# Optimization experiments

Measured on AMD Instinct MI355X. Metric: run time of the kernel, lower is better.

The kernel has to match this reference:

```python
import jax, jax.numpy as jnp
import numpy as np

B, L, E, H = 2, 2048, 1024, 16
D = E // H

def setup_inputs() -> dict:
    key = jax.random.key(0)
    ks = jax.random.split(key, 6)
    values = jax.random.normal(ks[0], (B, L, E), dtype=jnp.float32)
    keys = jax.random.normal(ks[1], (B, L, E), dtype=jnp.float32)
    query = jax.random.normal(ks[2], (B, L, E), dtype=jnp.float32)
    mask = jax.random.randint(ks[3], (B, 1, L, L), 0, 2, dtype=jnp.int32)
    W_out = jax.random.normal(ks[4], (E, E), dtype=jnp.float32) * 0.02
    b_out = jax.random.normal(ks[5], (E,), dtype=jnp.float32) * 0.02
    return {"values": values, "keys": keys, "query": query, "mask": mask,
            "W_out": W_out, "b_out": b_out}

def reference(values, keys, query, mask, W_out, b_out):
    # Note: source module never applies its per-head q/k/v Linear layers;
    # it only reshapes inputs, so we do the same.
    b, l, e = query.shape
    v = values.reshape(b, l, H, D)   # [B, K, H, D]
    k = keys.reshape(b, l, H, D)     # [B, K, H, D]
    q = query.reshape(b, l, H, D)    # [B, Q, H, D]
    # scores[b,h,q,k] = sum_d q[b,q,h,d] * k[b,k,h,d]
    scores = jnp.einsum('bqhd,bkhd->bhqk', q, k)
    scores = jnp.where(mask == 0, jnp.float32(-1e20), scores)
    # source scales by 1/sqrt(embed_size), not head_dim
    attn = jax.nn.softmax(scores / jnp.float32(E ** 0.5), axis=3)
    out = jnp.einsum('bhqk,bkhd->bqhd', attn, v).reshape(b, l, e)
    out = out @ W_out.T + b_out  # torch Linear: x @ W^T + b
    return out
```

## Files before the change

### kernel.cpp

```cpp
#include <hip/hip_runtime.h>
#include <hip/hip_bf16.h>

typedef __bf16 bf16;
typedef __bf16 bf16x8 __attribute__((ext_vector_type(8)));
typedef __bf16 bf16x4 __attribute__((ext_vector_type(4)));
typedef float  f32x4  __attribute__((ext_vector_type(4)));

#define B_ 2
#define L_ 2048
#define E_ 1024
#define H_ 16
#define D_ 64

__device__ __forceinline__ int swz(int r, int c) {
    return r * 64 + (((c ^ (r & 7)) & 7) << 3);
}

__global__ __launch_bounds__(256) void prep_kernel(const float* __restrict__ v,
                                                   const int* __restrict__ mask,
                                                   const float* __restrict__ W,
                                                   bf16* __restrict__ vt,
                                                   unsigned short* __restrict__ mt,
                                                   bf16* __restrict__ wb) {
    __shared__ __attribute__((aligned(16))) char sbuf[9216];
    const int bid = blockIdx.x;
    const int t = threadIdx.x;
    if (bid < 1024) {
        bf16* tile = (bf16*)sbuf;
        int bh = bid >> 5, b = bh >> 4, h = bh & 15;
        int k0 = (bid & 31) * 64;
        int kk = t >> 2, d0 = (t & 3) * 16;
        const float* src = v + (((size_t)(b * L_ + k0 + kk)) * H_ + h) * D_ + d0;
        float4 f[4];
#pragma unroll
        for (int i = 0; i < 4; i++) f[i] = reinterpret_cast<const float4*>(src)[i];
#pragma unroll
        for (int i = 0; i < 16; i++) {
            float val = reinterpret_cast<const float*>(f)[i];
            tile[(d0 + i) * 72 + kk] = (bf16)val;
        }
        __syncthreads();
        int dd = t >> 2, c = (t & 3) * 16;
        bf16* dst = vt + ((size_t)bh * 64 + dd) * 2048 + k0 + c;
        *reinterpret_cast<uint4*>(dst)     = *reinterpret_cast<const uint4*>(&tile[dd * 72 + c]);
        *reinterpret_cast<uint4*>(dst + 8) = *reinterpret_cast<const uint4*>(&tile[dd * 72 + c + 8]);
    } else if (bid < 3072) {
        unsigned char* tile = (unsigned char*)sbuf;
        int idx = bid - 1024;
        int b = idx >> 10, k0 = ((idx >> 5) & 31) * 64, q0 = (idx & 31) * 64;
        int qq = t >> 2, kc = (t & 3) * 16;
        const int* src = mask + (size_t)b * L_ * L_ + (size_t)(q0 + qq) * L_ + k0 + kc;
        int4 m[4];
#pragma unroll
        for (int i = 0; i < 4; i++) m[i] = reinterpret_cast<const int4*>(src)[i];
#pragma unroll
        for (int i = 0; i < 16; i++)
            tile[(kc + i) * 80 + qq] = (unsigned char)reinterpret_cast<const int*>(m)[i];
        __syncthreads();
        int kk = t >> 2, q16 = (t & 3) * 16;
        unsigned int bits = 0;
#pragma unroll
        for (int i = 0; i < 16; i++)
            bits |= ((unsigned int)(tile[kk * 80 + q16 + i] & 1)) << i;
        mt[((size_t)(b * L_) + k0 + kk) * (L_ / 16) + (q0 >> 4) + (t & 3)] = (unsigned short)bits;
    } else {
        int widx = bid - 3072;
#pragma unroll
        for (int j = 0; j < 16; j++) {
            int i = widx * 4096 + j * 256 + t;
            float4 f = reinterpret_cast<const float4*>(W)[i];
            bf16x4 o;
            o.x = (bf16)f.x; o.y = (bf16)f.y; o.z = (bf16)f.z; o.w = (bf16)f.w;
            reinterpret_cast<bf16x4*>(wb)[i] = o;
        }
    }
}

__global__ __launch_bounds__(256, 4) void attn_kernel(const float* __restrict__ q_,
                                                      const float* __restrict__ k_,
                                                      const bf16* __restrict__ vt,
                                                      const unsigned int* __restrict__ mt,
                                                      bf16* __restrict__ xb) {
    __shared__ __attribute__((aligned(16))) char smem[27136];
    bf16* Ks = (bf16*)smem;
    bf16* Vs = (bf16*)(smem + 8192);
    bf16* Ps = (bf16*)(smem + 16384);
    bf16* Qs = (bf16*)(smem + 16384);
    unsigned int* Ms32 = (unsigned int*)(smem + 26624);
    float* Om = (float*)smem;

    const int bh = blockIdx.y, b = bh >> 4, h = bh & 15;
    const int q0 = blockIdx.x * 64;
    const int t = threadIdx.x;
    const int w = t >> 6, lane = t & 63, quad = lane >> 4, ln = lane & 15;
    const int wq = w & 1, wk = w >> 1;
    const int r_ = t >> 2, cc = t & 3;

    const float CSCALE = 1.4426950408889634f / 32.0f;

    {
        const float* src = q_ + (((size_t)(b * L_ + q0 + r_)) * H_ + h) * D_ + cc * 16;
        float4 f[4];
#pragma unroll
        for (int i = 0; i < 4; i++) f[i] = reinterpret_cast<const float4*>(src)[i];
        bf16 tmp[16];
#pragma unroll
        for (int i = 0; i < 16; i++)
            tmp[i] = (bf16)(reinterpret_cast<const float*>(f)[i] * CSCALE);
        *reinterpret_cast<uint4*>(&Qs[swz(r_, cc * 2)])     = *reinterpret_cast<const uint4*>(&tmp[0]);
        *reinterpret_cast<uint4*>(&Qs[swz(r_, cc * 2 + 1)]) = *reinterpret_cast<const uint4*>(&tmp[8]);
    }
    __syncthreads();

    bf16x8 aq[2][2];
#pragma unroll
    for (int mi = 0; mi < 2; mi++)
#pragma unroll
        for (int dc = 0; dc < 2; dc++)
            aq[mi][dc] = *reinterpret_cast<const bf16x8*>(&Qs[swz(wq * 32 + mi * 16 + ln, dc * 4 + quad)]);

    f32x4 o[2][4], lf[2];
    const f32x4 zero = {0.f, 0.f, 0.f, 0.f};
#pragma unroll
    for (int mi = 0; mi < 2; mi++) {
        lf[mi] = zero;
#pragma unroll
        for (int di = 0; di < 4; di++) o[mi][di] = zero;
    }
    bf16x8 ones;
#pragma unroll
    for (int i = 0; i < 8; i++) ones[i] = (bf16)1.0f;

    bf16* Pw = Ps + w * 1280;

    for (int kt = 0; kt < L_ / 64; kt++) {
        const int k0 = kt * 64;
        {
            const float* ksrc = k_ + (((size_t)(b * L_ + k0 + r_)) * H_ + h) * D_ + cc * 16;
            float4 f[4];
#pragma unroll
            for (int i = 0; i < 4; i++) f[i] = reinterpret_cast<const float4*>(ksrc)[i];
            bf16 tmp[16];
#pragma unroll
            for (int i = 0; i < 16; i++)
                tmp[i] = (bf16)reinterpret_cast<const float*>(f)[i];
            *reinterpret_cast<uint4*>(&Ks[swz(r_, cc * 2)])     = *reinterpret_cast<const uint4*>(&tmp[0]);
            *reinterpret_cast<uint4*>(&Ks[swz(r_, cc * 2 + 1)]) = *reinterpret_cast<const uint4*>(&tmp[8]);
            const bf16* vsrc = vt + ((size_t)bh * 64 + r_) * 2048 + k0 + cc * 16;
            *reinterpret_cast<uint4*>(&Vs[swz(r_, cc * 2)])     = *reinterpret_cast<const uint4*>(vsrc);
            *reinterpret_cast<uint4*>(&Vs[swz(r_, cc * 2 + 1)]) = *reinterpret_cast<const uint4*>(vsrc + 8);
            if (t < 128) {
                int k = t >> 1, half = t & 1;
                Ms32[k * 2 + half] = mt[((size_t)(b * L_) + k0 + k) * (L_ / 32) + (q0 >> 5) + half];
            }
        }
        __syncthreads();

        f32x4 s[2][2];
#pragma unroll
        for (int mi = 0; mi < 2; mi++)
#pragma unroll
            for (int ni = 0; ni < 2; ni++) s[mi][ni] = zero;
#pragma unroll
        for (int ni = 0; ni < 2; ni++) {
#pragma unroll
            for (int dc = 0; dc < 2; dc++) {
                bf16x8 bk = *reinterpret_cast<const bf16x8*>(&Ks[swz(wk * 32 + ni * 16 + ln, dc * 4 + quad)]);
#pragma unroll
                for (int mi = 0; mi < 2; mi++)
                    s[mi][ni] = __builtin_amdgcn_mfma_f32_16x16x32_bf16(aq[mi][dc], bk, s[mi][ni], 0, 0, 0);
            }
        }

#pragma unroll
        for (int ni = 0; ni < 2; ni++) {
            unsigned int mw = Ms32[(wk * 32 + ni * 16 + ln) * 2 + wq];
#pragma unroll
            for (int mi = 0; mi < 2; mi++) {
#pragma unroll
                for (int r = 0; r < 4; r++) {
                    float p = __builtin_amdgcn_exp2f(s[mi][ni][r]) *
                              (float)((mw >> (mi * 16 + quad * 4 + r)) & 1u);
                    Pw[(mi * 16 + quad * 4 + r) * 40 + ni * 16 + ln] = (bf16)p;
                }
            }
        }

        bf16x8 ap[2];
#pragma unroll
        for (int mi = 0; mi < 2; mi++)
            ap[mi] = *reinterpret_cast<const bf16x8*>(&Pw[(mi * 16 + ln) * 40 + quad * 8]);
#pragma unroll
        for (int di = 0; di < 4; di++) {
            bf16x8 bv = *reinterpret_cast<const bf16x8*>(&Vs[swz(di * 16 + ln, wk * 4 + quad)]);
#pragma unroll
            for (int mi = 0; mi < 2; mi++)
                o[mi][di] = __builtin_amdgcn_mfma_f32_16x16x32_bf16(ap[mi], bv, o[mi][di], 0, 0, 0);
        }
#pragma unroll
        for (int mi = 0; mi < 2; mi++)
            lf[mi] = __builtin_amdgcn_mfma_f32_16x16x32_bf16(ap[mi], ones, lf[mi], 0, 0, 0);
        __syncthreads();
    }

    if (wk == 1) {
#pragma unroll
        for (int mi = 0; mi < 2; mi++) {
#pragma unroll
            for (int di = 0; di < 4; di++)
#pragma unroll
                for (int r = 0; r < 4; r++)
                    Om[(wq * 32 + mi * 16 + quad * 4 + r) * 68 + di * 16 + ln] = o[mi][di][r];
            if (ln == 0)
#pragma unroll
                for (int r = 0; r < 4; r++)
                    Om[(wq * 32 + mi * 16 + quad * 4 + r) * 68 + 64] = lf[mi][r];
        }
    }
    __syncthreads();
    if (wk == 0) {
#pragma unroll
        for (int mi = 0; mi < 2; mi++) {
            float lt[4];
#pragma unroll
            for (int r = 0; r < 4; r++)
                lt[r] = 1.0f / (lf[mi][r] + Om[(wq * 32 + mi * 16 + quad * 4 + r) * 68 + 64]);
#pragma unroll
            for (int di = 0; di < 4; di++)
#pragma unroll
                for (int r = 0; r < 4; r++) {
                    int q = wq * 32 + mi * 16 + quad * 4 + r;
                    float val = (o[mi][di][r] + Om[q * 68 + di * 16 + ln]) * lt[r];
                    xb[((size_t)(b * L_ + q0 + q)) * E_ + h * 64 + di * 16 + ln] = (bf16)val;
                }
        }
    }
}

__global__ __launch_bounds__(256, 4) void proj_kernel(const bf16* __restrict__ xb,
                                                      const bf16* __restrict__ wb,
                                                      const float* __restrict__ bias,
                                                      float* __restrict__ out) {
    __shared__ __attribute__((aligned(16))) bf16 As[64 * 64];
    __shared__ __attribute__((aligned(16))) bf16 Bs[64 * 64];
    const int n0 = blockIdx.x * 64, m0 = blockIdx.y * 64;
    const int t = threadIdx.x;
    const int w = t >> 6, lane = t & 63, quad = lane >> 4, ln = lane & 15;
    const int wm = w >> 1, wn = w & 1;
    const int r_ = t >> 1, c2 = (t & 1) * 4;

    f32x4 c[2][2];
    const f32x4 zero = {0.f, 0.f, 0.f, 0.f};
#pragma unroll
    for (int mi = 0; mi < 2; mi++)
#pragma unroll
        for (int ni = 0; ni < 2; ni++) c[mi][ni] = zero;

    for (int kt = 0; kt < E_ / 64; kt++) {
        const int k0 = kt * 64;
        {
            const bf16* asrc = xb + (size_t)(m0 + (t >> 2)) * E_ + k0 + (t & 3) * 16;
            const bf16* bsrc = wb + (size_t)(n0 + (t >> 2)) * E_ + k0 + (t & 3) * 16;
            int rr = t >> 2, c4 = (t & 3) * 2;
            *reinterpret_cast<uint4*>(&As[swz(rr, c4)])     = *reinterpret_cast<const uint4*>(asrc);
            *reinterpret_cast<uint4*>(&As[swz(rr, c4 + 1)]) = *reinterpret_cast<const uint4*>(asrc + 8);
            *reinterpret_cast<uint4*>(&Bs[swz(rr, c4)])     = *reinterpret_cast<const uint4*>(bsrc);
            *reinterpret_cast<uint4*>(&Bs[swz(rr, c4 + 1)]) = *reinterpret_cast<const uint4*>(bsrc + 8);
        }
        __syncthreads();
#pragma unroll
        for (int kc = 0; kc < 2; kc++) {
            bf16x8 a[2], bb[2];
#pragma unroll
            for (int mi = 0; mi < 2; mi++)
                a[mi] = *reinterpret_cast<const bf16x8*>(&As[swz(wm * 32 + mi * 16 + ln, kc * 4 + quad)]);
#pragma unroll
            for (int ni = 0; ni < 2; ni++)
                bb[ni] = *reinterpret_cast<const bf16x8*>(&Bs[swz(wn * 32 + ni * 16 + ln, kc * 4 + quad)]);
#pragma unroll
            for (int mi = 0; mi < 2; mi++)
#pragma unroll
                for (int ni = 0; ni < 2; ni++)
                    c[mi][ni] = __builtin_amdgcn_mfma_f32_16x16x32_bf16(a[mi], bb[ni], c[mi][ni], 0, 0, 0);
        }
        __syncthreads();
    }
#pragma unroll
    for (int ni = 0; ni < 2; ni++) {
        float bv = bias[n0 + wn * 32 + ni * 16 + ln];
#pragma unroll
        for (int mi = 0; mi < 2; mi++)
#pragma unroll
            for (int r = 0; r < 4; r++) {
                int row = m0 + wm * 32 + mi * 16 + quad * 4 + r;
                int col = n0 + wn * 32 + ni * 16 + ln;
                out[(size_t)row * E_ + col] = c[mi][ni][r] + bv;
            }
    }
}

extern "C" void kernel_launch(void* const* d_in, const int* in_sizes, int n_in,
                              void* d_out, int out_size, void* d_ws, size_t ws_size,
                              hipStream_t stream) {
    (void)in_sizes; (void)n_in; (void)out_size; (void)ws_size;
    const float* values = (const float*)d_in[0];
    const float* keys   = (const float*)d_in[1];
    const float* query  = (const float*)d_in[2];
    const int*   mask   = (const int*)d_in[3];
    const float* W_out  = (const float*)d_in[4];
    const float* b_out  = (const float*)d_in[5];
    float* out = (float*)d_out;

    char* ws = (char*)d_ws;
    bf16* vt = (bf16*)(ws);
    bf16* wb = (bf16*)(ws + 8388608);
    unsigned short* mt = (unsigned short*)(ws + 10485760);
    bf16* xb = (bf16*)(ws + 11534336);

    prep_kernel<<<3136, 256, 0, stream>>>(values, mask, W_out, vt, mt, wb);
    attn_kernel<<<dim3(L_ / 64, B_ * H_), 256, 0, stream>>>(query, keys, vt, (const unsigned int*)mt, xb);
    proj_kernel<<<dim3(E_ / 64, (B_ * L_) / 64), 256, 0, stream>>>(xb, wb, b_out, out);
}
```

Baseline: 218.1 us.

## Rework attention with 32x32 MFMA, register P exchange, prefetch, and bf16 K prep

Attention now uses 32x32x16 bf16 MFMAs with S transposed, so P moves between lane halves through permlane32 swaps instead of an LDS round trip. It also prefetches the next K/V/mask tile into registers and sums row weights on the scalar path instead of with a ones-MFMA. Keys are converted to bf16 once in the prep kernel, and the mask is packed with a wave ballot into a q-major bit layout. Output is staged through LDS for coalesced stores, at the cost of extra prep work and different register pressure.

Measured after the change: 213.0 us. 1.02x faster.

```diff
diff --git a/kernel.cpp b/kernel.cpp
--- a/kernel.cpp
+++ b/kernel.cpp
@@ -5,6 +5,7 @@
 typedef __bf16 bf16x8 __attribute__((ext_vector_type(8)));
 typedef __bf16 bf16x4 __attribute__((ext_vector_type(4)));
 typedef float  f32x4  __attribute__((ext_vector_type(4)));
+typedef float  f32x16 __attribute__((ext_vector_type(16)));
 
 #define B_ 2
 #define L_ 2048
@@ -16,17 +17,29 @@
     return r * 64 + (((c ^ (r & 7)) & 7) << 3);
 }
 
+__device__ __forceinline__ float swap_half(float x, int h) {
+#if __has_builtin(__builtin_amdgcn_permlane32_swap)
+    typedef unsigned int u32x2 __attribute__((ext_vector_type(2)));
+    unsigned int xu = __builtin_bit_cast(unsigned int, x);
+    u32x2 r = __builtin_amdgcn_permlane32_swap(xu, xu, false, false);
+    return __builtin_bit_cast(float, h ? r.x : r.y);
+#else
+    return __shfl(x, (((int)threadIdx.x) & 63) ^ 32, 64);
+#endif
+}
+
 __global__ __launch_bounds__(256) void prep_kernel(const float* __restrict__ v,
+                                                   const float* __restrict__ keys,
                                                    const int* __restrict__ mask,
                                                    const float* __restrict__ W,
                                                    bf16* __restrict__ vt,
-                                                   unsigned short* __restrict__ mt,
+                                                   bf16* __restrict__ kb,
+                                                   unsigned int* __restrict__ mtq2,
                                                    bf16* __restrict__ wb) {
-    __shared__ __attribute__((aligned(16))) char sbuf[9216];
+    __shared__ __attribute__((aligned(16))) bf16 tile[64 * 72];
     const int bid = blockIdx.x;
     const int t = threadIdx.x;
     if (bid < 1024) {
-        bf16* tile = (bf16*)sbuf;
         int bh = bid >> 5, b = bh >> 4, h = bh & 15;
         int k0 = (bid & 31) * 64;
         int kk = t >> 2, d0 = (t & 3) * 16;
@@ -35,36 +48,38 @@
 #pragma unroll
         for (int i = 0; i < 4; i++) f[i] = reinterpret_cast<const float4*>(src)[i];
 #pragma unroll
-        for (int i = 0; i < 16; i++) {
-            float val = reinterpret_cast<const float*>(f)[i];
-            tile[(d0 + i) * 72 + kk] = (bf16)val;
-        }
+        for (int i = 0; i < 16; i++)
+            tile[(d0 + i) * 72 + kk] = (bf16)reinterpret_cast<const float*>(f)[i];
         __syncthreads();
         int dd = t >> 2, c = (t & 3) * 16;
         bf16* dst = vt + ((size_t)bh * 64 + dd) * 2048 + k0 + c;
         *reinterpret_cast<uint4*>(dst)     = *reinterpret_cast<const uint4*>(&tile[dd * 72 + c]);
         *reinterpret_cast<uint4*>(dst + 8) = *reinterpret_cast<const uint4*>(&tile[dd * 72 + c + 8]);
-    } else if (bid < 3072) {
-        unsigned char* tile = (unsigned char*)sbuf;
+    } else if (bid < 2048) {
         int idx = bid - 1024;
-        int b = idx >> 10, k0 = ((idx >> 5) & 31) * 64, q0 = (idx & 31) * 64;
-        int qq = t >> 2, kc = (t & 3) * 16;
-        const int* src = mask + (size_t)b * L_ * L_ + (size_t)(q0 + qq) * L_ + k0 + kc;
-        int4 m[4];
-#pragma unroll
-        for (int i = 0; i < 4; i++) m[i] = reinterpret_cast<const int4*>(src)[i];
-#pragma unroll
-        for (int i = 0; i < 16; i++)
-            tile[(kc + i) * 80 + qq] = (unsigned char)reinterpret_cast<const int*>(m)[i];
-        __syncthreads();
-        int kk = t >> 2, q16 = (t & 3) * 16;
-        unsigned int bits = 0;
-#pragma unroll
-        for (int i = 0; i < 16; i++)
-            bits |= ((unsigned int)(tile[kk * 80 + q16 + i] & 1)) << i;
-        mt[((size_t)(b * L_) + k0 + kk) * (L_ / 16) + (q0 >> 4) + (t & 3)] = (unsigned short)bits;
+        int b = idx >> 9;
+        int q = (idx & 511) * 4 + (t >> 6);
+        int li = t & 63;
+        const int* mrow = mask + ((size_t)b * L_ + q) * L_;
+        unsigned int* mq = mtq2 + (size_t)b * 64 * 2048;
+        for (int pass = 0; pass < 32; pass++) {
+            int m = mrow[pass * 64 + li];
+            unsigned long long bal = __ballot(m & 1);
+            if (li == 0) mq[(size_t)(pass * 2) * 2048 + q] = (unsigned int)bal;
+            if (li == 1) mq[(size_t)(pass * 2 + 1) * 2048 + q] = (unsigned int)(bal >> 32);
+        }
+    } else if (bid < 2560) {
+        int idx = bid - 2048;
+#pragma unroll
+        for (int j = 0; j < 8; j++) {
+            int i = idx * 2048 + j * 256 + t;
+            float4 f = reinterpret_cast<const float4*>(keys)[i];
+            bf16x4 o;
+            o.x = (bf16)f.x; o.y = (bf16)f.y; o.z = (bf16)f.z; o.w = (bf16)f.w;
+            reinterpret_cast<bf16x4*>(kb)[i] = o;
+        }
     } else {
-        int widx = bid - 3072;
+        int widx = bid - 2560;
 #pragma unroll
         for (int j = 0; j < 16; j++) {
             int i = widx * 4096 + j * 256 + t;
@@ -77,29 +92,30 @@
 }
 
 __global__ __launch_bounds__(256, 4) void attn_kernel(const float* __restrict__ q_,
-                                                      const float* __restrict__ k_,
+                                                      const bf16* __restrict__ kb,
                                                       const bf16* __restrict__ vt,
-                                                      const unsigned int* __restrict__ mt,
+                                                      const unsigned int* __restrict__ mtq2,
                                                       bf16* __restrict__ xb) {
     __shared__ __attribute__((aligned(16))) char smem[27136];
     bf16* Ks = (bf16*)smem;
     bf16* Vs = (bf16*)(smem + 8192);
-    bf16* Ps = (bf16*)(smem + 16384);
     bf16* Qs = (bf16*)(smem + 16384);
-    unsigned int* Ms32 = (unsigned int*)(smem + 26624);
+    unsigned int* Ms32 = (unsigned int*)(smem + 24576);
     float* Om = (float*)smem;
-
-    const int bh = blockIdx.y, b = bh >> 4, h = bh & 15;
+    float* Lrow = (float*)(smem + 16384);
+    bf16* Xs = (bf16*)(smem + 17408);
+
+    const int bh = blockIdx.y, b = bh >> 4, hd = bh & 15;
     const int q0 = blockIdx.x * 64;
     const int t = threadIdx.x;
-    const int w = t >> 6, lane = t & 63, quad = lane >> 4, ln = lane & 15;
+    const int w = t >> 6, lane = t & 63, h = lane >> 5, l31 = lane & 31;
     const int wq = w & 1, wk = w >> 1;
-    const int r_ = t >> 2, cc = t & 3;
+    const int r_ = t >> 2, cq = t & 3;
 
     const float CSCALE = 1.4426950408889634f / 32.0f;
 
     {
-        const float* src = q_ + (((size_t)(b * L_ + q0 + r_)) * H_ + h) * D_ + cc * 16;
+        const float* src = q_ + ((size_t)(b * L_ + q0 + r_)) * E_ + hd * 64 + cq * 16;
         float4 f[4];
 #pragma unroll
         for (int i = 0; i < 4; i++) f[i] = reinterpret_cast<const float4*>(src)[i];
@@ -107,133 +123,131 @@
 #pragma unroll
         for (int i = 0; i < 16; i++)
             tmp[i] = (bf16)(reinterpret_cast<const float*>(f)[i] * CSCALE);
-        *reinterpret_cast<uint4*>(&Qs[swz(r_, cc * 2)])     = *reinterpret_cast<const uint4*>(&tmp[0]);
-        *reinterpret_cast<uint4*>(&Qs[swz(r_, cc * 2 + 1)]) = *reinterpret_cast<const uint4*>(&tmp[8]);
+        *reinterpret_cast<uint4*>(&Qs[swz(r_, cq * 2)])     = *reinterpret_cast<const uint4*>(&tmp[0]);
+        *reinterpret_cast<uint4*>(&Qs[swz(r_, cq * 2 + 1)]) = *reinterpret_cast<const uint4*>(&tmp[8]);
+
+        const bf16* ksrc = kb + ((size_t)(b * L_ + r_)) * E_ + hd * 64 + cq * 16;
+        *reinterpret_cast<uint4*>(&Ks[swz(r_, cq * 2)])     = *reinterpret_cast<const uint4*>(ksrc);
+        *reinterpret_cast<uint4*>(&Ks[swz(r_, cq * 2 + 1)]) = *reinterpret_cast<const uint4*>(ksrc + 8);
+        const bf16* vsrc = vt + ((size_t)bh * 64 + r_) * 2048 + cq * 16;
+        *reinterpret_cast<uint4*>(&Vs[swz(r_, cq * 2)])     = *reinterpret_cast<const uint4*>(vsrc);
+        *reinterpret_cast<uint4*>(&Vs[swz(r_, cq * 2 + 1)]) = *reinterpret_cast<const uint4*>(vsrc + 8);
+        if (t < 128)
+            Ms32[t] = mtq2[(size_t)(b * 64 + (t >> 6)) * 2048 + q0 + (t & 63)];
     }
     __syncthreads();
 
-    bf16x8 aq[2][2];
-#pragma unroll
-    for (int mi = 0; mi < 2; mi++)
-#pragma unroll
-        for (int dc = 0; dc < 2; dc++)
-            aq[mi][dc] = *reinterpret_cast<const bf16x8*>(&Qs[swz(wq * 32 + mi * 16 + ln, dc * 4 + quad)]);
-
-    f32x4 o[2][4], lf[2];
-    const f32x4 zero = {0.f, 0.f, 0.f, 0.f};
-#pragma unroll
-    for (int mi = 0; mi < 2; mi++) {
-        lf[mi] = zero;
-#pragma unroll
-        for (int di = 0; di < 4; di++) o[mi][di] = zero;
-    }
-    bf16x8 ones;
-#pragma unroll
-    for (int i = 0; i < 8; i++) ones[i] = (bf16)1.0f;
-
-    bf16* Pw = Ps + w * 1280;
+    bf16x8 bq[4];
+#pragma unroll
+    for (int dc = 0; dc < 4; dc++)
+        bq[dc] = *reinterpret_cast<const bf16x8*>(&Qs[swz(wq * 32 + l31, dc * 2 + h)]);
+
+    f32x16 oc[2] = {{}, {}};
+    float lsum = 0.0f;
 
     for (int kt = 0; kt < L_ / 64; kt++) {
-        const int k0 = kt * 64;
-        {
-            const float* ksrc = k_ + (((size_t)(b * L_ + k0 + r_)) * H_ + h) * D_ + cc * 16;
-            float4 f[4];
-#pragma unroll
-            for (int i = 0; i < 4; i++) f[i] = reinterpret_cast<const float4*>(ksrc)[i];
-            bf16 tmp[16];
-#pragma unroll
-            for (int i = 0; i < 16; i++)
-                tmp[i] = (bf16)reinterpret_cast<const float*>(f)[i];
-            *reinterpret_cast<uint4*>(&Ks[swz(r_, cc * 2)])     = *reinterpret_cast<const uint4*>(&tmp[0]);
-            *reinterpret_cast<uint4*>(&Ks[swz(r_, cc * 2 + 1)]) = *reinterpret_cast<const uint4*>(&tmp[8]);
-            const bf16* vsrc = vt + ((size_t)bh * 64 + r_) * 2048 + k0 + cc * 16;
-            *reinterpret_cast<uint4*>(&Vs[swz(r_, cc * 2)])     = *reinterpret_cast<const uint4*>(vsrc);
-            *reinterpret_cast<uint4*>(&Vs[swz(r_, cc * 2 + 1)]) = *reinterpret_cast<const uint4*>(vsrc + 8);
-            if (t < 128) {
-                int k = t >> 1, half = t & 1;
-                Ms32[k * 2 + half] = mt[((size_t)(b * L_) + k0 + k) * (L_ / 32) + (q0 >> 5) + half];
-            }
-        }
-        __syncthreads();
-
-        f32x4 s[2][2];
-#pragma unroll
-        for (int mi = 0; mi < 2; mi++)
-#pragma unroll
-            for (int ni = 0; ni < 2; ni++) s[mi][ni] = zero;
-#pragma unroll
-        for (int ni = 0; ni < 2; ni++) {
-#pragma unroll
-            for (int dc = 0; dc < 2; dc++) {
-                bf16x8 bk = *reinterpret_cast<const bf16x8*>(&Ks[swz(wk * 32 + ni * 16 + ln, dc * 4 + quad)]);
-#pragma unroll
-                for (int mi = 0; mi < 2; mi++)
-                    s[mi][ni] = __builtin_amdgcn_mfma_f32_16x16x32_bf16(aq[mi][dc], bk, s[mi][ni], 0, 0, 0);
-            }
-        }
-
-#pragma unroll
-        for (int ni = 0; ni < 2; ni++) {
-            unsigned int mw = Ms32[(wk * 32 + ni * 16 + ln) * 2 + wq];
-#pragma unroll
-            for (int mi = 0; mi < 2; mi++) {
-#pragma unroll
-                for (int r = 0; r < 4; r++) {
-                    float p = __builtin_amdgcn_exp2f(s[mi][ni][r]) *
-                              (float)((mw >> (mi * 16 + quad * 4 + r)) & 1u);
-                    Pw[(mi * 16 + quad * 4 + r) * 40 + ni * 16 + ln] = (bf16)p;
-                }
-            }
-        }
-
-        bf16x8 ap[2];
-#pragma unroll
-        for (int mi = 0; mi < 2; mi++)
-            ap[mi] = *reinterpret_cast<const bf16x8*>(&Pw[(mi * 16 + ln) * 40 + quad * 8]);
-#pragma unroll
-        for (int di = 0; di < 4; di++) {
-            bf16x8 bv = *reinterpret_cast<const bf16x8*>(&Vs[swz(di * 16 + ln, wk * 4 + quad)]);
-#pragma unroll
-            for (int mi = 0; mi < 2; mi++)
-                o[mi][di] = __builtin_amdgcn_mfma_f32_16x16x32_bf16(ap[mi], bv, o[mi][di], 0, 0, 0);
-        }
-#pragma unroll
-        for (int mi = 0; mi < 2; mi++)
-            lf[mi] = __builtin_amdgcn_mfma_f32_16x16x32_bf16(ap[mi], ones, lf[mi], 0, 0, 0);
-        __syncthreads();
-    }
+        uint4 kn0, kn1, vn0, vn1;
+        unsigned int mn = 0;
+        const bool hasn = (kt + 1) < L_ / 64;
+        if (hasn) {
+            const int kn = (kt + 1) * 64;
+            const bf16* ksrc = kb + ((size_t)(b * L_ + kn + r_)) * E_ + hd * 64 + cq * 16;
+            kn0 = *reinterpret_cast<const uint4*>(ksrc);
+            kn1 = *reinterpret_cast<const uint4*>(ksrc + 8);
+            const bf16* vsrc = vt + ((size_t)bh * 64 + r_) * 2048 + kn + cq * 16;
+            vn0 = *reinterpret_cast<const uint4*>(vsrc);
+            vn1 = *reinterpret_cast<const uint4*>(vsrc + 8);
+            if (t < 128)
+                mn = mtq2[(size_t)(b * 64 + (kt + 1) * 2 + (t >> 6)) * 2048 + q0 + (t & 63)];
+        }
+
+        f32x16 st = {};
+#pragma unroll
+        for (int dc = 0; dc < 4; dc++) {
+            bf16x8 ak = *reinterpret_cast<const bf16x8*>(&Ks[swz(wk * 32 + l31, dc * 2 + h)]);
+            st = __builtin_amdgcn_mfma_f32_32x32x16_bf16(ak, bq[dc], st, 0, 0, 0);
+        }
+
+        const unsigned int mwh = Ms32[wk * 64 + wq * 32 + l31] >> (h * 4);
+        float pv[16];
+#pragma unroll
+        for (int i = 0; i < 16; i++) {
+            const int base = (i & 3) + 8 * (i >> 2);
+            float e = __builtin_amdgcn_exp2f(st[i]);
+            pv[i] = ((mwh >> base) & 1u) ? e : 0.0f;
+            lsum += pv[i];
+        }
+
+        bf16x8 bp[2];
+#pragma unroll
+        for (int kc = 0; kc < 2; kc++) {
+            const int gA = kc * 2, gB = gA + 1;
+            float lo[4], hi[4];
+#pragma unroll
+            for (int r = 0; r < 4; r++) {
+                float own  = h ? pv[gB * 4 + r] : pv[gA * 4 + r];
+                float send = h ? pv[gA * 4 + r] : pv[gB * 4 + r];
+                float recv = swap_half(send, h);
+                lo[r] = h ? recv : own;
+                hi[r] = h ? own : recv;
+            }
+            bf16x8 bb;
+#pragma unroll
+            for (int r = 0; r < 4; r++) { bb[r] = (bf16)lo[r]; bb[4 + r] = (bf16)hi[r]; }
+            bp[kc] = bb;
+        }
+
+#pragma unroll
+        for (int da = 0; da < 2; da++)
+#pragma unroll
+            for (int kc = 0; kc < 2; kc++) {
+                bf16x8 av = *reinterpret_cast<const bf16x8*>(&Vs[swz(da * 32 + l31, wk * 4 + kc * 2 + h)]);
+                oc[da] = __builtin_amdgcn_mfma_f32_32x32x16_bf16(av, bp[kc], oc[da], 0, 0, 0);
+            }
+
+        __syncthreads();
+        if (hasn) {
+            *reinterpret_cast<uint4*>(&Ks[swz(r_, cq * 2)])     = kn0;
+            *reinterpret_cast<uint4*>(&Ks[swz(r_, cq * 2 + 1)]) = kn1;
+            *reinterpret_cast<uint4*>(&Vs[swz(r_, cq * 2)])     = vn0;
+            *reinterpret_cast<uint4*>(&Vs[swz(r_, cq * 2 + 1)]) = vn1;
+            if (t < 128) Ms32[t] = mn;
+        }
+        __syncthreads();
+    }
+
+    float lw = lsum + swap_half(lsum, h);
 
     if (wk == 1) {
 #pragma unroll
-        for (int mi = 0; mi < 2; mi++) {
-#pragma unroll
-            for (int di = 0; di < 4; di++)
-#pragma unroll
-                for (int r = 0; r < 4; r++)
-                    Om[(wq * 32 + mi * 16 + quad * 4 + r) * 68 + di * 16 + ln] = o[mi][di][r];
-            if (ln == 0)
-#pragma unroll
-                for (int r = 0; r < 4; r++)
-                    Om[(wq * 32 + mi * 16 + quad * 4 + r) * 68 + 64] = lf[mi][r];
-        }
+        for (int da = 0; da < 2; da++)
+#pragma unroll
+            for (int i = 0; i < 16; i++) {
+                int d = da * 32 + (i & 3) + 8 * (i >> 2) + 4 * h;
+                Om[d * 64 + wq * 32 + l31] = oc[da][i];
+            }
+        if (h == 0) Lrow[wq * 32 + l31] = lw;
     }
     __syncthreads();
     if (wk == 0) {
-#pragma unroll
-        for (int mi = 0; mi < 2; mi++) {
-            float lt[4];
-#pragma unroll
-            for (int r = 0; r < 4; r++)
-                lt[r] = 1.0f / (lf[mi][r] + Om[(wq * 32 + mi * 16 + quad * 4 + r) * 68 + 64]);
-#pragma unroll
-            for (int di = 0; di < 4; di++)
-#pragma unroll
-                for (int r = 0; r < 4; r++) {
-                    int q = wq * 32 + mi * 16 + quad * 4 + r;
-                    float val = (o[mi][di][r] + Om[q * 68 + di * 16 + ln]) * lt[r];
-                    xb[((size_t)(b * L_ + q0 + q)) * E_ + h * 64 + di * 16 + ln] = (bf16)val;
-                }
-        }
+        float rinv = 1.0f / (lw + Lrow[wq * 32 + l31]);
+#pragma unroll
+        for (int da = 0; da < 2; da++)
+#pragma unroll
+            for (int g = 0; g < 4; g++) {
+                int d0 = da * 32 + 8 * g + 4 * h;
+                bf16x4 pk;
+#pragma unroll
+                for (int r = 0; r < 4; r++)
+                    pk[r] = (bf16)((oc[da][g * 4 + r] + Om[(d0 + r) * 64 + wq * 32 + l31]) * rinv);
+                *reinterpret_cast<bf16x4*>(&Xs[(wq * 32 + l31) * 72 + d0]) = pk;
+            }
+    }
+    __syncthreads();
+    {
+        bf16* dst = xb + ((size_t)(b * L_ + q0 + r_)) * E_ + hd * 64 + cq * 16;
+        *reinterpret_cast<uint4*>(dst)     = *reinterpret_cast<const uint4*>(&Xs[r_ * 72 + cq * 16]);
+        *reinterpret_cast<uint4*>(dst + 8) = *reinterpret_cast<const uint4*>(&Xs[r_ * 72 + cq * 16 + 8]);
     }
 }
 
@@ -247,7 +261,6 @@
     const int t = threadIdx.x;
     const int w = t >> 6, lane = t & 63, quad = lane >> 4, ln = lane & 15;
     const int wm = w >> 1, wn = w & 1;
-    const int r_ = t >> 1, c2 = (t & 1) * 4;
 
     f32x4 c[2][2];
     const f32x4 zero = {0.f, 0.f, 0.f, 0.f};
@@ -312,12 +325,13 @@
     float* out = (float*)d_out;
 
     char* ws = (char*)d_ws;
-    bf16* vt = (bf16*)(ws);
-    bf16* wb = (bf16*)(ws + 8388608);
-    unsigned short* mt = (unsigned short*)(ws + 10485760);
-    bf16* xb = (bf16*)(ws + 11534336);
-
-    prep_kernel<<<3136, 256, 0, stream>>>(values, mask, W_out, vt, mt, wb);
-    attn_kernel<<<dim3(L_ / 64, B_ * H_), 256, 0, stream>>>(query, keys, vt, (const unsigned int*)mt, xb);
+    bf16* kb = (bf16*)(ws);
+    bf16* vt = (bf16*)(ws + 8388608);
+    bf16* wb = (bf16*)(ws + 16777216);
+    unsigned int* mtq2 = (unsigned int*)(ws + 18874368);
+    bf16* xb = (bf16*)(ws + 19922944);
+
+    prep_kernel<<<2624, 256, 0, stream>>>(values, keys, mask, W_out, vt, kb, mtq2, wb);
+    attn_kernel<<<dim3(L_ / 64, B_ * H_), 256, 0, stream>>>(query, kb, vt, mtq2, xb);
     proj_kernel<<<dim3(E_ / 64, (B_ * L_) / 64), 256, 0, stream>>>(xb, wb, b_out, out);
 }
```
